# Kernel tuning notes

Hardware: AMD Instinct MI355X
Metric: run time of the kernel (lower is better)

## Reference

```python
import jax, jax.numpy as jnp
import numpy as np

N_HEADS = 8
EPS = 1e-5


def setup_inputs() -> dict:
    key = jax.random.key(0)
    ks = jax.random.split(key, 5)
    c = 512
    x = jax.random.normal(ks[0], (2, c, 2, 32, 32), dtype=jnp.float32)
    s = 0.02
    Wq = jax.random.normal(ks[1], (c, c), dtype=jnp.float32) * s
    Wk = jax.random.normal(ks[2], (c, c), dtype=jnp.float32) * s
    Wv = jax.random.normal(ks[3], (c, c), dtype=jnp.float32) * s
    Wo = jax.random.normal(ks[4], (c, c), dtype=jnp.float32) * s
    bo = jnp.zeros((c,), dtype=jnp.float32)
    gamma = jnp.ones((c,), dtype=jnp.float32)
    beta = jnp.zeros((c,), dtype=jnp.float32)
    return {"x": x, "Wq": Wq, "Wk": Wk, "Wv": Wv, "Wo": Wo, "bo": bo,
            "gamma": gamma, "beta": beta}


def reference(x, Wq, Wk, Wv, Wo, bo, gamma, beta):
    b, c, d, h, w = x.shape
    seq = d * h * w
    # [b, c, d, h, w] -> [b, seq, c]
    xs = jnp.transpose(x, (0, 2, 3, 4, 1)).reshape(b, seq, c)
    # LayerNorm over channel dim
    mu = jnp.mean(xs, axis=-1, keepdims=True)
    var = jnp.mean(jnp.square(xs - mu), axis=-1, keepdims=True)
    xn = (xs - mu) * jax.lax.rsqrt(var + EPS) * gamma + beta
    # Self-attention (cond falls back to x); weights stored [in, out]
    dh = c // N_HEADS
    q = (xn @ Wq).reshape(b, seq, N_HEADS, dh)
    k = (xn @ Wk).reshape(b, seq, N_HEADS, dh)
    v = (xn @ Wv).reshape(b, seq, N_HEADS, dh)
    scale = dh ** (-0.5)
    attn = jnp.einsum('bihd,bjhd->bhij', q, k) * scale  # [b, H, seq, seq]
    attn = jax.nn.softmax(attn, axis=-1)
    out = jnp.einsum('bhij,bjhd->bihd', attn, v).reshape(b, seq, c)
    out = out @ Wo + bo
    y = out + xs  # residual
    return jnp.transpose(y.reshape(b, d, h, w, c), (0, 4, 1, 2, 3))
```

## Files before the change

kernel.cpp:

```cpp
#include <hip/hip_runtime.h>
#include <cstdint>

typedef unsigned short u16;
typedef unsigned char u8;
typedef __bf16 bf16x8 __attribute__((ext_vector_type(8)));
typedef float f32x4 __attribute__((ext_vector_type(4)));
typedef u16 u16x4 __attribute__((ext_vector_type(4)));
typedef u16 u16x8 __attribute__((ext_vector_type(8)));

__device__ __forceinline__ u16 f2bf(float f) {
  union { float f; unsigned u; } v; v.f = f;
  unsigned r = v.u + 0x7FFFu + ((v.u >> 16) & 1u);
  return (u16)(r >> 16);
}

__device__ __forceinline__ float bf2f(u16 u) {
  union { unsigned u; float f; } c; c.u = ((unsigned)u) << 16;
  return c.f;
}

__device__ __forceinline__ f32x4 mfma16(bf16x8 a, bf16x8 b, f32x4 c) {
  return __builtin_amdgcn_mfma_f32_16x16x32_bf16(a, b, c, 0, 0, 0);
}

__device__ __forceinline__ f32x4 mfma8(long a, long b, f32x4 c) {
  return __builtin_amdgcn_mfma_f32_16x16x32_fp8_fp8(a, b, c, 0, 0, 0);
}

__device__ __forceinline__ u8 f2fp8(float f) {
  return (u8)(__builtin_amdgcn_cvt_pk_fp8_f32(f, f, 0, false) & 0xff);
}

__device__ __forceinline__ void gload_lds16(const void* g, void* l) {
  auto* lp = reinterpret_cast<__attribute__((address_space(3))) unsigned int*>(
      reinterpret_cast<uintptr_t>(l));
  const auto* gp = reinterpret_cast<const __attribute__((address_space(1))) unsigned int*>(
      reinterpret_cast<uintptr_t>(g));
  __builtin_amdgcn_global_load_lds(gp, lp, 16, 0, 0);
}

template <int N>
__device__ __forceinline__ void waitcnt_vm() {
  if constexpr (N == 0)      asm volatile("s_waitcnt vmcnt(0)" ::: "memory");
  else if constexpr (N == 2) asm volatile("s_waitcnt vmcnt(2)" ::: "memory");
  else if constexpr (N == 4) asm volatile("s_waitcnt vmcnt(4)" ::: "memory");
  else if constexpr (N == 6) asm volatile("s_waitcnt vmcnt(6)" ::: "memory");
  else                       asm volatile("s_waitcnt vmcnt(8)" ::: "memory");
}

__global__ __launch_bounds__(256) void prep_kernel(const float* __restrict__ Wq,
                                                   const float* __restrict__ Wk,
                                                   const float* __restrict__ Wv,
                                                   const float* __restrict__ Wo,
                                                   const float* __restrict__ x,
                                                   const float* __restrict__ gamma,
                                                   const float* __restrict__ beta,
                                                   u16* __restrict__ wt_out,
                                                   u16* __restrict__ xn) {
  struct LnSh {
    float red0[32][8];
    float red1[32][8];
    float mu[8], rs[8];
    u16 tile[8][520];
  };
  struct WtSh { float tile[32][33]; };
  __shared__ __align__(16) char shraw[sizeof(LnSh) > sizeof(WtSh) ? sizeof(LnSh) : sizeof(WtSh)];
  int bid = blockIdx.x;
  int t = threadIdx.x;
  if (bid < 512) {
    LnSh& S = *reinterpret_cast<LnSh*>(shraw);
    int b = bid >> 8;
    int s0 = (bid & 255) * 8;
    int tx = t & 7, ty = t >> 3;
    const float* xb = x + (size_t)b * 512 * 2048 + s0 + tx;
    float vals[16];
    float sum = 0.f, sq = 0.f;
#pragma unroll
    for (int k = 0; k < 16; k++) {
      float v = xb[(size_t)(ty + k * 32) * 2048];
      vals[k] = v;
      sum += v; sq += v * v;
    }
    S.red0[ty][tx] = sum; S.red1[ty][tx] = sq;
    __syncthreads();
    if (t < 8) {
      float a = 0.f, c2 = 0.f;
#pragma unroll
      for (int i = 0; i < 32; i++) { a += S.red0[i][t]; c2 += S.red1[i][t]; }
      float mu = a * (1.f / 512.f);
      float var = c2 * (1.f / 512.f) - mu * mu;
      S.mu[t] = mu;
      S.rs[t] = rsqrtf(var + 1e-5f);
    }
    __syncthreads();
    float mu = S.mu[tx], rs = S.rs[tx];
#pragma unroll
    for (int k = 0; k < 16; k++) {
      int ch = ty + k * 32;
      S.tile[tx][ch] = f2bf((vals[k] - mu) * rs * gamma[ch] + beta[ch]);
    }
    __syncthreads();
    int col = (t & 63) * 8;
    int r0 = t >> 6;
    u16* outb = xn + (size_t)(b * 2048 + s0) * 512;
#pragma unroll
    for (int i = 0; i < 2; i++) {
      int row = r0 + 4 * i;
      *(u16x8*)(outb + (size_t)row * 512 + col) = *(const u16x8*)(&S.tile[row][col]);
    }
  } else {
    WtSh& S = *reinterpret_cast<WtSh*>(shraw);
    int wid = bid - 512;
    int z = wid >> 8;
    const float* W = (z == 0) ? Wq : (z == 1) ? Wk : (z == 2) ? Wv : Wo;
    u16* o = wt_out + (size_t)z * 262144;
    int rem = wid & 255;
    int n0 = (rem >> 4) * 32, k0 = (rem & 15) * 32;
    int tx = t & 31, ty = t >> 5;
#pragma unroll
    for (int i = 0; i < 4; i++)
      S.tile[ty + i * 8][tx] = W[(size_t)(k0 + ty + i * 8) * 512 + n0 + tx];
    __syncthreads();
#pragma unroll
    for (int i = 0; i < 4; i++) {
      int n = ty + i * 8;
      o[(size_t)(n0 + n) * 512 + k0 + tx] = f2bf(S.tile[tx][n]);
    }
  }
}

template <int AM, int AN>
__device__ __forceinline__ void gemm_tile_ring(const u16* __restrict__ A, const u16* __restrict__ B,
                                               int m0, int n0, f32x4 acc[AM][AN],
                                               u16* As, u16* Bs) {
  constexpr int BM = AM * 32, BN = AN * 32;
  constexpr int LA = BM / 64, LB = BN / 64;
  constexpr int L = LA + LB;
  int t = threadIdx.x;
  int w = t >> 6, lane = t & 63;
  int wm = w >> 1, wn = w & 1;
  int arow = t >> 2;
  int acol = (t & 3) * 8;
  int lrow = lane & 15;
  int lko = (lane >> 4) * 8;

  auto stage = [&](int buf, int k0) {
#pragma unroll
    for (int g = 0; g < LA; ++g)
      gload_lds16(A + (size_t)(m0 + g * 64 + arow) * 512 + k0 + acol,
                  As + buf * (BM * 32) + g * 2048 + w * 512);
#pragma unroll
    for (int g = 0; g < LB; ++g)
      gload_lds16(B + (size_t)(n0 + g * 64 + arow) * 512 + k0 + acol,
                  Bs + buf * (BN * 32) + g * 2048 + w * 512);
  };

  stage(0, 0);
  stage(1, 32);
  stage(2, 64);
  __syncthreads();

  for (int tt = 0; tt < 16; ++tt) {
    int pk = (tt + 3 < 16) ? (tt + 3) * 32 : 0;
    stage((tt + 3) & 3, pk);
    const u16* as = As + (tt & 3) * (BM * 32);
    const u16* bs = Bs + (tt & 3) * (BN * 32);
    bf16x8 af[AM], bfr[AN];
#pragma unroll
    for (int i = 0; i < AM; i++) af[i] = *(const bf16x8*)(as + (wm * (AM * 16) + i * 16 + lrow) * 32 + lko);
#pragma unroll
    for (int j = 0; j < AN; j++) bfr[j] = *(const bf16x8*)(bs + (wn * (AN * 16) + j * 16 + lrow) * 32 + lko);
    __builtin_amdgcn_s_setprio(1);
#pragma unroll
    for (int i = 0; i < AM; i++)
#pragma unroll
      for (int j = 0; j < AN; j++)
        acc[i][j] = mfma16(af[i], bfr[j], acc[i][j]);
    __builtin_amdgcn_s_setprio(0);
    waitcnt_vm<2 * L>();
    __builtin_amdgcn_s_barrier();
  }
  waitcnt_vm<0>();
}

__global__ __launch_bounds__(256) void gemm_qkv(const u16* __restrict__ xn, const u16* __restrict__ wt,
                                                u8* __restrict__ Qb, u8* __restrict__ Kp,
                                                u8* __restrict__ Vp) {
  __shared__ u16 As[4 * 64 * 32];
  __shared__ u16 Bs[4 * 128 * 32];
  const float SCQ = 0.125f * 1.4426950408889634f;
  int mat = blockIdx.z;
  const u16* WT = wt + (size_t)mat * 262144;
  int m0 = blockIdx.x * 64, n0 = blockIdx.y * 128;
  f32x4 acc[2][4] = {};
  gemm_tile_ring<2, 4>(xn, WT, m0, n0, acc, As, Bs);
  int t = threadIdx.x, w = t >> 6, lane = t & 63;
  int wm = w >> 1, wn = w & 1, lrow = lane & 15, lgrp = lane >> 4;
#pragma unroll
  for (int i = 0; i < 2; i++) {
#pragma unroll
    for (int j = 0; j < 4; j++) {
      int gr0 = m0 + wm * 32 + i * 16 + lgrp * 4;
      int gc = n0 + wn * 64 + j * 16 + lrow;
      if (mat == 0) {
#pragma unroll
        for (int r = 0; r < 4; r++)
          Qb[(size_t)(gr0 + r) * 512 + gc] = f2fp8(acc[i][j][r] * SCQ);
      } else if (mat == 1) {
        int h = gc >> 6, d = gc & 63;
        int half = d >> 5, lg = (d >> 3) & 3, jj = d & 7;
#pragma unroll
        for (int r = 0; r < 4; r++) {
          int kg = gr0 + r;
          int bq = kg >> 11, kl = kg & 2047;
          int kt = kl >> 5, kw = kl & 31;
          int tt = (kw >> 2) & 1;
          int kwb = kw - 4 * tt;
          int lr = ((kwb >> 3) << 2) | (kwb & 3);
          int c = 2 * tt + half;
          size_t idx = ((size_t)((bq * 8 + h) * 64 + kt) * 4 + c) * 512 + (lg * 16 + lr) * 8 + jj;
          Kp[idx] = f2fp8(acc[i][j][r]);
        }
      } else {
        int h = gc >> 6, d = gc & 63;
        int dt = d >> 4, lr = d & 15;
        int kg = gr0;
        int bq = kg >> 11, kl = kg & 2047;
        int kt = kl >> 5, kw = kl & 31;
        int lg = kw >> 3, j0 = kw & 7;
        unsigned u = __builtin_amdgcn_cvt_pk_fp8_f32(acc[i][j][0], acc[i][j][1], 0, false);
        u = __builtin_amdgcn_cvt_pk_fp8_f32(acc[i][j][2], acc[i][j][3], u, true);
        size_t idx = ((size_t)((bq * 8 + h) * 64 + kt) * 4 + dt) * 512 + (lg * 16 + lr) * 8 + j0;
        *(unsigned*)(Vp + idx) = u;
      }
    }
  }
}

__global__ __launch_bounds__(256, 4) void attn_kernel(const u8* __restrict__ Qb, const u8* __restrict__ Kp,
                                                      const u8* __restrict__ Vp, u16* __restrict__ Opart,
                                                      float* __restrict__ ml, int logS) {
  int S = 1 << logS;
  int bid = blockIdx.x;
  int qt = bid >> (4 + logS);
  int group = bid & (16 * S - 1);
  int hb = group >> logS, sp = group & (S - 1);
  int b = hb >> 3, h = hb & 7;
  int kt0 = sp * (64 >> logS);
  int nsteps = 64 >> logS;

  int t = threadIdx.x, w = t >> 6, lane = t & 63;
  int lrow = lane & 15, lgrp = lane >> 4, lko = lgrp * 8;
  int q0 = qt * 128 + w * 32;

  const u8* Qp = Qb + (size_t)(b * 2048 + q0 + lrow) * 512 + h * 64 + lko;
  long qa0 = *(const long*)(Qp);
  long qa1 = *(const long*)(Qp + 32);
  long qb0 = *(const long*)(Qp + 16 * 512);
  long qb1 = *(const long*)(Qp + 16 * 512 + 32);

  const u8* Kbh = Kp + (size_t)hb * 131072 + lane * 8;
  const u8* Vbh = Vp + (size_t)hb * 131072 + lane * 8;

  f32x4 acca[4] = {}, accb[4] = {};
  float lsum_a = 0.f, lsum_b = 0.f;

  long kA[4], vA[4], kB[4], vB[4];

  auto loadKV = [&](long* kf, long* vf, int st) {
    const u8* pk = Kbh + (size_t)(kt0 + st) * 2048;
    const u8* pv = Vbh + (size_t)(kt0 + st) * 2048;
#pragma unroll
    for (int c = 0; c < 4; c++) kf[c] = *(const long*)(pk + c * 512);
#pragma unroll
    for (int c = 0; c < 4; c++) vf[c] = *(const long*)(pv + c * 512);
  };

  auto computeStep = [&](const long* kc, const long* vc) {
    f32x4 sa0 = {}, sa1 = {}, sb0 = {}, sb1 = {};
    __builtin_amdgcn_s_setprio(1);
    sa0 = mfma8(kc[0], qa0, sa0);
    sa0 = mfma8(kc[1], qa1, sa0);
    sa1 = mfma8(kc[2], qa0, sa1);
    sa1 = mfma8(kc[3], qa1, sa1);
    sb0 = mfma8(kc[0], qb0, sb0);
    sb0 = mfma8(kc[1], qb1, sb0);
    sb1 = mfma8(kc[2], qb0, sb1);
    sb1 = mfma8(kc[3], qb1, sb1);
    __builtin_amdgcn_s_setprio(0);

    float pa[8], pb8[8];
#pragma unroll
    for (int jj = 0; jj < 4; jj++) pa[jj] = exp2f(sa0[jj]);
#pragma unroll
    for (int jj = 0; jj < 4; jj++) pa[4 + jj] = exp2f(sa1[jj]);
#pragma unroll
    for (int jj = 0; jj < 4; jj++) pb8[jj] = exp2f(sb0[jj]);
#pragma unroll
    for (int jj = 0; jj < 4; jj++) pb8[4 + jj] = exp2f(sb1[jj]);
    lsum_a += ((pa[0] + pa[1]) + (pa[2] + pa[3])) + ((pa[4] + pa[5]) + (pa[6] + pa[7]));
    lsum_b += ((pb8[0] + pb8[1]) + (pb8[2] + pb8[3])) + ((pb8[4] + pb8[5]) + (pb8[6] + pb8[7]));

    unsigned alo = __builtin_amdgcn_cvt_pk_fp8_f32(pa[0], pa[1], 0, false);
    alo = __builtin_amdgcn_cvt_pk_fp8_f32(pa[2], pa[3], alo, true);
    unsigned ahi = __builtin_amdgcn_cvt_pk_fp8_f32(pa[4], pa[5], 0, false);
    ahi = __builtin_amdgcn_cvt_pk_fp8_f32(pa[6], pa[7], ahi, true);
    long pla = (long)(((unsigned long long)ahi << 32) | alo);
    unsigned blo = __builtin_amdgcn_cvt_pk_fp8_f32(pb8[0], pb8[1], 0, false);
    blo = __builtin_amdgcn_cvt_pk_fp8_f32(pb8[2], pb8[3], blo, true);
    unsigned bhi = __builtin_amdgcn_cvt_pk_fp8_f32(pb8[4], pb8[5], 0, false);
    bhi = __builtin_amdgcn_cvt_pk_fp8_f32(pb8[6], pb8[7], bhi, true);
    long plb = (long)(((unsigned long long)bhi << 32) | blo);

    __builtin_amdgcn_s_setprio(1);
    acca[0] = mfma8(pla, vc[0], acca[0]);
    acca[1] = mfma8(pla, vc[1], acca[1]);
    acca[2] = mfma8(pla, vc[2], acca[2]);
    acca[3] = mfma8(pla, vc[3], acca[3]);
    accb[0] = mfma8(plb, vc[0], accb[0]);
    accb[1] = mfma8(plb, vc[1], accb[1]);
    accb[2] = mfma8(plb, vc[2], accb[2]);
    accb[3] = mfma8(plb, vc[3], accb[3]);
    __builtin_amdgcn_s_setprio(0);
  };

  loadKV(kA, vA, 0);
  for (int st = 0; st < nsteps; st += 2) {
    loadKV(kB, vB, (st + 1 < nsteps) ? st + 1 : 0);
    computeStep(kA, vA);
    loadKV(kA, vA, (st + 2 < nsteps) ? st + 2 : 0);
    computeStep(kB, vB);
  }

  lsum_a += __shfl_xor(lsum_a, 16); lsum_a += __shfl_xor(lsum_a, 32);
  lsum_b += __shfl_xor(lsum_b, 16); lsum_b += __shfl_xor(lsum_b, 32);

  if (lgrp == 0) {
    int row = b * 2048 + q0 + lrow;
    ml[(size_t)sp * 32768 + row * 8 + h] = lsum_a;
    ml[(size_t)sp * 32768 + (row + 16) * 8 + h] = lsum_b;
  }

  u16* Ao = Opart + (size_t)sp * 2097152 + (size_t)(b * 2048 + q0) * 512 + h * 64;
#pragma unroll
  for (int r = 0; r < 4; r++) {
#pragma unroll
    for (int dt = 0; dt < 4; dt++) {
      Ao[(size_t)(lgrp * 4 + r) * 512 + dt * 16 + lrow] = f2bf(acca[dt][r]);
      Ao[(size_t)(16 + lgrp * 4 + r) * 512 + dt * 16 + lrow] = f2bf(accb[dt][r]);
    }
  }
}

template <int S>
__global__ __launch_bounds__(256) void attn_combine(const u16* __restrict__ Opart,
                                                    const float* __restrict__ ml,
                                                    u16* __restrict__ AO) {
  int gid = blockIdx.x * 256 + threadIdx.x;
  int pair = gid >> 3, dcol = (gid & 7) * 8;
  int row = pair >> 3, h = pair & 7;
  float lsum = 0.f;
#pragma unroll
  for (int s = 0; s < S; s++) lsum += ml[(size_t)s * 32768 + pair];
  float inv = 1.0f / lsum;
  float o[8] = {};
#pragma unroll
  for (int s = 0; s < S; s++) {
    u16x8 ov = *(const u16x8*)(Opart + (size_t)s * 2097152 + (size_t)row * 512 + h * 64 + dcol);
#pragma unroll
    for (int j = 0; j < 8; j++) o[j] += bf2f(ov[j]);
  }
  u16x8 outv;
#pragma unroll
  for (int j = 0; j < 8; j++) outv[j] = f2bf(o[j] * inv);
  *(u16x8*)(AO + (size_t)row * 512 + h * 64 + dcol) = outv;
}

__global__ __launch_bounds__(256) void gemm_out(const u16* __restrict__ AO, const u16* __restrict__ WoT,
                                                const float* __restrict__ bo, const float* __restrict__ x,
                                                float* __restrict__ y) {
  __shared__ u16 As[4 * 64 * 32];
  __shared__ u16 Bs[4 * 64 * 32];
  int m0 = blockIdx.x * 64, n0 = blockIdx.y * 64;
  f32x4 acc[2][2] = {};
  gemm_tile_ring<2, 2>(AO, WoT, m0, n0, acc, As, Bs);
  int t = threadIdx.x, w = t >> 6, lane = t & 63;
  int wm = w >> 1, wn = w & 1, lrow = lane & 15, lgrp = lane >> 4;
#pragma unroll
  for (int i = 0; i < 2; i++) {
#pragma unroll
    for (int j = 0; j < 2; j++) {
      int gr0 = m0 + wm * 32 + i * 16 + lgrp * 4;
      int gc = n0 + wn * 32 + j * 16 + lrow;
      int bb = gr0 >> 11, s = gr0 & 2047;
      float bias = bo[gc];
      const float* xp = x + ((size_t)bb * 512 + gc) * 2048 + s;
      float4 xv = *(const float4*)xp;
      float4 o;
      o.x = acc[i][j][0] + bias + xv.x;
      o.y = acc[i][j][1] + bias + xv.y;
      o.z = acc[i][j][2] + bias + xv.z;
      o.w = acc[i][j][3] + bias + xv.w;
      *(float4*)(y + ((size_t)bb * 512 + gc) * 2048 + s) = o;
    }
  }
}

extern "C" void kernel_launch(void* const* d_in, const int* in_sizes, int n_in,
                              void* d_out, int out_size, void* d_ws, size_t ws_size,
                              hipStream_t stream) {
  const float* x = (const float*)d_in[0];
  const float* Wq = (const float*)d_in[1];
  const float* Wk = (const float*)d_in[2];
  const float* Wv = (const float*)d_in[3];
  const float* Wo = (const float*)d_in[4];
  const float* bo = (const float*)d_in[5];
  const float* gamma = (const float*)d_in[6];
  const float* beta = (const float*)d_in[7];
  float* y = (float*)d_out;
  char* ws = (char*)d_ws;
  u16* xn = (u16*)(ws);
  u16* wt = (u16*)(ws + (4 << 20));
  u8* Qb = (u8*)(ws + (6 << 20));
  u8* Kp = (u8*)(ws + (10 << 20));
  u8* Vp = (u8*)(ws + (14 << 20));
  u16* AO = (u16*)(ws + (18 << 20));
  float* ml = (float*)(ws + (22 << 20));
  u16* Opart = (u16*)(ws + (23 << 20));

  int logS;
  if (ws_size >= (40u << 20)) logS = 2;
  else if (ws_size >= (32u << 20)) logS = 1;
  else { logS = 0; Opart = AO; }

  prep_kernel<<<dim3(1536), dim3(256), 0, stream>>>(Wq, Wk, Wv, Wo, x, gamma, beta, wt, xn);
  gemm_qkv<<<dim3(64, 4, 3), dim3(256), 0, stream>>>(xn, wt, Qb, Kp, Vp);
  attn_kernel<<<dim3(256 << logS), dim3(256), 0, stream>>>(Qb, Kp, Vp, Opart, ml, logS);
  if (logS == 2)      attn_combine<4><<<dim3(1024), dim3(256), 0, stream>>>(Opart, ml, AO);
  else if (logS == 1) attn_combine<2><<<dim3(1024), dim3(256), 0, stream>>>(Opart, ml, AO);
  else                attn_combine<1><<<dim3(1024), dim3(256), 0, stream>>>(Opart, ml, AO);
  gemm_out<<<dim3(64, 8), dim3(256), 0, stream>>>(AO, wt + 3 * 262144, bo, x, y);
}
```

Measured before the change: 67.17 us.

## Fuse split-K attention combine into output GEMM and compute row sums via MFMA

Measured after the change: 71.54 us. +6.5%, slower.

```diff
diff --git a/kernel.cpp b/kernel.cpp
--- a/kernel.cpp
+++ b/kernel.cpp
@@ -240,6 +240,7 @@
 __global__ __launch_bounds__(256, 4) void attn_kernel(const u8* __restrict__ Qb, const u8* __restrict__ Kp,
                                                       const u8* __restrict__ Vp, u16* __restrict__ Opart,
                                                       float* __restrict__ ml, int logS) {
+  const long ONES8 = 0x3838383838383838L;
   int S = 1 << logS;
   int bid = blockIdx.x;
   int qt = bid >> (4 + logS);
@@ -263,7 +264,7 @@
   const u8* Vbh = Vp + (size_t)hb * 131072 + lane * 8;
 
   f32x4 acca[4] = {}, accb[4] = {};
-  float lsum_a = 0.f, lsum_b = 0.f;
+  f32x4 suma = {}, sumb = {};
 
   long kA[4], vA[4], kB[4], vB[4];
 
@@ -298,8 +299,6 @@
     for (int jj = 0; jj < 4; jj++) pb8[jj] = exp2f(sb0[jj]);
 #pragma unroll
     for (int jj = 0; jj < 4; jj++) pb8[4 + jj] = exp2f(sb1[jj]);
-    lsum_a += ((pa[0] + pa[1]) + (pa[2] + pa[3])) + ((pa[4] + pa[5]) + (pa[6] + pa[7]));
-    lsum_b += ((pb8[0] + pb8[1]) + (pb8[2] + pb8[3])) + ((pb8[4] + pb8[5]) + (pb8[6] + pb8[7]));
 
     unsigned alo = __builtin_amdgcn_cvt_pk_fp8_f32(pa[0], pa[1], 0, false);
     alo = __builtin_amdgcn_cvt_pk_fp8_f32(pa[2], pa[3], alo, true);
@@ -321,6 +320,8 @@
     accb[1] = mfma8(plb, vc[1], accb[1]);
     accb[2] = mfma8(plb, vc[2], accb[2]);
     accb[3] = mfma8(plb, vc[3], accb[3]);
+    suma = mfma8(pla, ONES8, suma);
+    sumb = mfma8(plb, ONES8, sumb);
     __builtin_amdgcn_s_setprio(0);
   };
 
@@ -332,13 +333,13 @@
     computeStep(kB, vB);
   }
 
-  lsum_a += __shfl_xor(lsum_a, 16); lsum_a += __shfl_xor(lsum_a, 32);
-  lsum_b += __shfl_xor(lsum_b, 16); lsum_b += __shfl_xor(lsum_b, 32);
-
-  if (lgrp == 0) {
-    int row = b * 2048 + q0 + lrow;
-    ml[(size_t)sp * 32768 + row * 8 + h] = lsum_a;
-    ml[(size_t)sp * 32768 + (row + 16) * 8 + h] = lsum_b;
+  if (lrow == 0) {
+    int rowa = b * 2048 + q0 + lgrp * 4;
+#pragma unroll
+    for (int r = 0; r < 4; r++) {
+      ml[(size_t)sp * 32768 + (rowa + r) * 8 + h] = suma[r];
+      ml[(size_t)sp * 32768 + (rowa + 16 + r) * 8 + h] = sumb[r];
+    }
   }
 
   u16* Ao = Opart + (size_t)sp * 2097152 + (size_t)(b * 2048 + q0) * 512 + h * 64;
@@ -353,39 +354,86 @@
 }
 
 template <int S>
-__global__ __launch_bounds__(256) void attn_combine(const u16* __restrict__ Opart,
-                                                    const float* __restrict__ ml,
-                                                    u16* __restrict__ AO) {
-  int gid = blockIdx.x * 256 + threadIdx.x;
-  int pair = gid >> 3, dcol = (gid & 7) * 8;
-  int row = pair >> 3, h = pair & 7;
-  float lsum = 0.f;
-#pragma unroll
-  for (int s = 0; s < S; s++) lsum += ml[(size_t)s * 32768 + pair];
-  float inv = 1.0f / lsum;
-  float o[8] = {};
-#pragma unroll
-  for (int s = 0; s < S; s++) {
-    u16x8 ov = *(const u16x8*)(Opart + (size_t)s * 2097152 + (size_t)row * 512 + h * 64 + dcol);
-#pragma unroll
-    for (int j = 0; j < 8; j++) o[j] += bf2f(ov[j]);
-  }
-  u16x8 outv;
-#pragma unroll
-  for (int j = 0; j < 8; j++) outv[j] = f2bf(o[j] * inv);
-  *(u16x8*)(AO + (size_t)row * 512 + h * 64 + dcol) = outv;
-}
-
-__global__ __launch_bounds__(256) void gemm_out(const u16* __restrict__ AO, const u16* __restrict__ WoT,
-                                                const float* __restrict__ bo, const float* __restrict__ x,
-                                                float* __restrict__ y) {
+__global__ __launch_bounds__(256) void gemm_out_fused(const u16* __restrict__ Opart,
+                                                      const float* __restrict__ ml,
+                                                      const u16* __restrict__ WoT,
+                                                      const float* __restrict__ bo,
+                                                      const float* __restrict__ x,
+                                                      float* __restrict__ y) {
   __shared__ u16 As[4 * 64 * 32];
   __shared__ u16 Bs[4 * 64 * 32];
+  __shared__ float invs[64][8];
   int m0 = blockIdx.x * 64, n0 = blockIdx.y * 64;
+  int t = threadIdx.x, w = t >> 6, lane = t & 63;
+  int arow = t >> 2;
+  int acol = (t & 3) * 8;
+  int lrow = lane & 15, lko = (lane >> 4) * 8;
+  int wm = w >> 1, wn = w & 1;
+
+  for (int e = t; e < 512; e += 256) {
+    int row = m0 + (e >> 3), hh = e & 7;
+    float s = 0.f;
+#pragma unroll
+    for (int si = 0; si < S; si++) s += ml[(size_t)si * 32768 + (size_t)row * 8 + hh];
+    invs[e >> 3][hh] = 1.0f / s;
+  }
+  __syncthreads();
+
+  u16x8 rA[S];
+  auto loadA = [&](int tile) {
+#pragma unroll
+    for (int si = 0; si < S; si++)
+      rA[si] = *(const u16x8*)(Opart + (size_t)si * 2097152 + (size_t)(m0 + arow) * 512 + tile * 32 + acol);
+  };
+  auto combineWrite = [&](int tile) {
+    float inv = invs[arow][tile >> 1];
+    u16x8 wv;
+#pragma unroll
+    for (int j = 0; j < 8; j++) {
+      float o = 0.f;
+#pragma unroll
+      for (int si = 0; si < S; si++) o += bf2f(rA[si][j]);
+      wv[j] = f2bf(o * inv);
+    }
+    *(u16x8*)(As + ((tile) & 3) * 2048 + t * 8) = wv;
+  };
+  auto stageB = [&](int tile) {
+    gload_lds16(WoT + (size_t)(n0 + arow) * 512 + tile * 32 + acol,
+                Bs + (tile & 3) * 2048 + w * 512);
+  };
+
+  loadA(0); combineWrite(0);
+  loadA(1); combineWrite(1);
+  loadA(2); combineWrite(2);
+  stageB(0); stageB(1); stageB(2);
+  __syncthreads();
+
   f32x4 acc[2][2] = {};
-  gemm_tile_ring<2, 2>(AO, WoT, m0, n0, acc, As, Bs);
-  int t = threadIdx.x, w = t >> 6, lane = t & 63;
-  int wm = w >> 1, wn = w & 1, lrow = lane & 15, lgrp = lane >> 4;
+  for (int tt = 0; tt < 16; ++tt) {
+    int nt = (tt + 3 < 16) ? tt + 3 : 0;
+    loadA(nt);
+    stageB(nt);
+    const u16* as = As + (tt & 3) * 2048;
+    const u16* bs = Bs + (tt & 3) * 2048;
+    bf16x8 af[2], bfr[2];
+#pragma unroll
+    for (int i = 0; i < 2; i++) af[i] = *(const bf16x8*)(as + (wm * 32 + i * 16 + lrow) * 32 + lko);
+#pragma unroll
+    for (int j = 0; j < 2; j++) bfr[j] = *(const bf16x8*)(bs + (wn * 32 + j * 16 + lrow) * 32 + lko);
+    __builtin_amdgcn_s_setprio(1);
+#pragma unroll
+    for (int i = 0; i < 2; i++)
+#pragma unroll
+      for (int j = 0; j < 2; j++)
+        acc[i][j] = mfma16(af[i], bfr[j], acc[i][j]);
+    __builtin_amdgcn_s_setprio(0);
+    combineWrite(nt);
+    asm volatile("s_waitcnt lgkmcnt(0)" ::: "memory");
+    __builtin_amdgcn_s_barrier();
+  }
+  waitcnt_vm<0>();
+
+  int lgrp = lane >> 4;
 #pragma unroll
   for (int i = 0; i < 2; i++) {
 #pragma unroll
@@ -424,20 +472,21 @@
   u8* Qb = (u8*)(ws + (6 << 20));
   u8* Kp = (u8*)(ws + (10 << 20));
   u8* Vp = (u8*)(ws + (14 << 20));
-  u16* AO = (u16*)(ws + (18 << 20));
   float* ml = (float*)(ws + (22 << 20));
   u16* Opart = (u16*)(ws + (23 << 20));
 
   int logS;
   if (ws_size >= (40u << 20)) logS = 2;
   else if (ws_size >= (32u << 20)) logS = 1;
-  else { logS = 0; Opart = AO; }
+  else { logS = 0; Opart = (u16*)(ws + (18 << 20)); }
 
   prep_kernel<<<dim3(1536), dim3(256), 0, stream>>>(Wq, Wk, Wv, Wo, x, gamma, beta, wt, xn);
   gemm_qkv<<<dim3(64, 4, 3), dim3(256), 0, stream>>>(xn, wt, Qb, Kp, Vp);
   attn_kernel<<<dim3(256 << logS), dim3(256), 0, stream>>>(Qb, Kp, Vp, Opart, ml, logS);
-  if (logS == 2)      attn_combine<4><<<dim3(1024), dim3(256), 0, stream>>>(Opart, ml, AO);
-  else if (logS == 1) attn_combine<2><<<dim3(1024), dim3(256), 0, stream>>>(Opart, ml, AO);
-  else                attn_combine<1><<<dim3(1024), dim3(256), 0, stream>>>(Opart, ml, AO);
-  gemm_out<<<dim3(64, 8), dim3(256), 0, stream>>>(AO, wt + 3 * 262144, bo, x, y);
-}
+  if (logS == 2)
+    gemm_out_fused<4><<<dim3(64, 8), dim3(256), 0, stream>>>(Opart, ml, wt + 3 * 262144, bo, x, y);
+  else if (logS == 1)
+    gemm_out_fused<2><<<dim3(64, 8), dim3(256), 0, stream>>>(Opart, ml, wt + 3 * 262144, bo, x, y);
+  else
+    gemm_out_fused<1><<<dim3(64, 8), dim3(256), 0, stream>>>(Opart, ml, wt + 3 * 262144, bo, x, y);
+}
```
